# Kernel optimization log

Hardware: AMD Instinct MI355X
Metric: run time of the kernel (lower is better)

The kernel has to match this reference:

```python
import jax, jax.numpy as jnp
import numpy as np

ANG = 5  # angRes; n = ANG*ANG
EPS = 1e-12  # torch F.normalize eps

def _l2norm(x, axis):
    n = jnp.sqrt(jnp.sum(x * x, axis=axis, keepdims=True))
    return x / jnp.maximum(n, EPS)

def setup_inputs() -> dict:
    key = jax.random.key(0)
    kq, kk, kv = jax.random.split(key, 3)
    shape = (16, 16, 25, 16, 128)  # b c n h w
    return {
        "token_q": jax.random.normal(kq, shape, dtype=jnp.float32),
        "token_k": jax.random.normal(kk, shape, dtype=jnp.float32),
        "token_v": jax.random.normal(kv, shape, dtype=jnp.float32),
    }

def reference(token_q, token_k, token_v):
    b, c, n, h, w = token_q.shape
    u = v = ANG
    buffer = token_v

    def to_q(x):  # b c (u v) h w -> b (c h) (w u v)
        return x.reshape(b, c, u, v, h, w).transpose(0, 1, 4, 5, 2, 3).reshape(b, c * h, w * u * v)

    def to_k(x):  # b c (u v) h w -> b (w u v) (c h)
        return x.reshape(b, c, u, v, h, w).transpose(0, 5, 2, 3, 1, 4).reshape(b, w * u * v, c * h)

    unfold_q = _l2norm(to_q(token_q), axis=-1)      # [b, ch, wuv]
    unfold_k = _l2norm(to_k(token_k), axis=-2)      # [b, wuv, ch]
    unfold_v = to_q(token_v)                        # [b, ch, wuv]

    att = jnp.einsum('bts,bsr->btr', unfold_q, unfold_k)  # [b, ch, ch]
    size = c * h
    causal = jnp.tril(jnp.ones((size, size), dtype=bool))
    att = jnp.where(causal, att, jnp.float32(-1e15))
    att = jax.nn.softmax(att, axis=-1)

    out = jnp.einsum('btr,brs->bts', att, unfold_v)  # [b, ch, wuv]
    # b (c h) (w u v) -> b c (u v) h w
    out = out.reshape(b, c, h, w, u, v).transpose(0, 1, 4, 5, 2, 3).reshape(b, c, n, h, w)
    return out + buffer
```

## Files before the change

### kernel.cpp

```cpp
#include <hip/hip_runtime.h>
#include <math.h>

#define SB 819200
#define SC 51200
#define SN 2048
#define CH 256
#define NW 3200
#define NPARTS 10
#define PARTLEN 320
#define NCHUNK 5
#define SPART 1048576
#define G1BLOCKS 480

typedef __bf16 bf16x8 __attribute__((ext_vector_type(8)));
typedef __bf16 bf16x4 __attribute__((ext_vector_type(4)));
typedef __bf16 bf16x2 __attribute__((ext_vector_type(2)));
typedef float  f32x4  __attribute__((ext_vector_type(4)));

__device__ __forceinline__ bf16x8 cvt8(float4 a, float4 b) {
    bf16x8 r;
    r[0] = (__bf16)a.x; r[1] = (__bf16)a.y; r[2] = (__bf16)a.z; r[3] = (__bf16)a.w;
    r[4] = (__bf16)b.x; r[5] = (__bf16)b.y; r[6] = (__bf16)b.z; r[7] = (__bf16)b.w;
    return r;
}

__device__ __forceinline__ float dot4(float4 a) {
    return a.x * a.x + a.y * a.y + a.z * a.z + a.w * a.w;
}

__global__ __launch_bounds__(256, 2) void gemm1_kernel(const float* __restrict__ q,
                                                       const float* __restrict__ k,
                                                       float* __restrict__ Sp,
                                                       float* __restrict__ nq2p,
                                                       float* __restrict__ nk2p) {
    __shared__ alignas(16) __bf16 As[128 * 72];
    __shared__ alignas(16) __bf16 Bs[128 * 72];

    const int tid = threadIdx.x;
    const int lane = tid & 63;
    const int wave = tid >> 6;

    const int bx = blockIdx.x;
    const int tile = bx % 3;
    const int part = (bx / 3) % NPARTS;
    const int b = bx / (3 * NPARTS);
    const int tm = (tile + 1) >> 1;
    const int tn = tile >> 1;

    const int wm = wave >> 1;
    const int wn = wave & 1;

    const int srow = tid >> 1;
    const int scol = (tid & 1) * 32;
    const int ta = tm * 128 + srow;
    const int rb = tn * 128 + srow;
    const float* qrow = q + (size_t)b * SB + (size_t)(ta >> 4) * SC + (size_t)(ta & 15) * 128;
    const float* krow = k + (size_t)b * SB + (size_t)(rb >> 4) * SC + (size_t)(rb & 15) * 128;

    const bool doQ = (tile != 2);
    const bool doK = (tile != 1);

    f32x4 acc[4][4] = {};
    bool live[4][4];
#pragma unroll
    for (int mi = 0; mi < 4; mi++)
#pragma unroll
        for (int ni = 0; ni < 4; ni++)
            live[mi][ni] = (tn * 128 + wn * 64 + ni * 16) <= (tm * 128 + wm * 64 + mi * 16);

    float sqa = 0.f, sqb = 0.f;
    float4 av[8], bv[8];

    {
        const int kg = part * PARTLEN;
        const size_t koff = (size_t)(kg >> 7) * SN + (kg & 127) + scol;
#pragma unroll
        for (int j = 0; j < 8; j++) {
            av[j] = *(const float4*)(qrow + koff + j * 4);
            bv[j] = *(const float4*)(krow + koff + j * 4);
        }
#pragma unroll
        for (int j = 0; j < 4; j++) {
            *(bf16x8*)&As[srow * 72 + scol + j * 8] = cvt8(av[2 * j], av[2 * j + 1]);
            *(bf16x8*)&Bs[srow * 72 + scol + j * 8] = cvt8(bv[2 * j], bv[2 * j + 1]);
        }
        if (doQ) {
#pragma unroll
            for (int j = 0; j < 8; j++) sqa += dot4(av[j]);
        }
        if (doK) {
#pragma unroll
            for (int j = 0; j < 8; j++) sqb += dot4(bv[j]);
        }
    }
    __syncthreads();

    for (int ch = 0; ch < NCHUNK; ch++) {
        if (ch < NCHUNK - 1) {
            const int kg = part * PARTLEN + (ch + 1) * 64;
            const size_t koff = (size_t)(kg >> 7) * SN + (kg & 127) + scol;
#pragma unroll
            for (int j = 0; j < 8; j++) {
                av[j] = *(const float4*)(qrow + koff + j * 4);
                bv[j] = *(const float4*)(krow + koff + j * 4);
            }
        }
#pragma unroll
        for (int ks = 0; ks < 2; ks++) {
            const int ko = ks * 32 + (lane >> 4) * 8;
            bf16x8 af[4], bf[4];
#pragma unroll
            for (int mi = 0; mi < 4; mi++)
                af[mi] = *(const bf16x8*)&As[(wm * 64 + mi * 16 + (lane & 15)) * 72 + ko];
#pragma unroll
            for (int ni = 0; ni < 4; ni++)
                bf[ni] = *(const bf16x8*)&Bs[(wn * 64 + ni * 16 + (lane & 15)) * 72 + ko];
#pragma unroll
            for (int mi = 0; mi < 4; mi++)
#pragma unroll
                for (int ni = 0; ni < 4; ni++)
                    if (live[mi][ni])
                        acc[mi][ni] = __builtin_amdgcn_mfma_f32_16x16x32_bf16(
                            af[mi], bf[ni], acc[mi][ni], 0, 0, 0);
        }
        if (ch < NCHUNK - 1) {
            __syncthreads();
#pragma unroll
            for (int j = 0; j < 4; j++) {
                *(bf16x8*)&As[srow * 72 + scol + j * 8] = cvt8(av[2 * j], av[2 * j + 1]);
                *(bf16x8*)&Bs[srow * 72 + scol + j * 8] = cvt8(bv[2 * j], bv[2 * j + 1]);
            }
            if (doQ) {
#pragma unroll
                for (int j = 0; j < 8; j++) sqa += dot4(av[j]);
            }
            if (doK) {
#pragma unroll
                for (int j = 0; j < 8; j++) sqb += dot4(bv[j]);
            }
            __syncthreads();
        }
    }

    float* o = Sp + (size_t)part * SPART + (size_t)b * 65536;
#pragma unroll
    for (int mi = 0; mi < 4; mi++)
#pragma unroll
        for (int ni = 0; ni < 4; ni++) {
            if (!live[mi][ni]) continue;
            const int r = tn * 128 + wn * 64 + ni * 16 + (lane & 15);
#pragma unroll
            for (int j = 0; j < 4; j++) {
                const int t = tm * 128 + wm * 64 + mi * 16 + (lane >> 4) * 4 + j;
                o[(size_t)t * 256 + r] = acc[mi][ni][j];
            }
        }

    sqa += __shfl_xor(sqa, 1, 64);
    sqb += __shfl_xor(sqb, 1, 64);
    if (!(lane & 1)) {
        if (doQ) nq2p[part * 4096 + b * 256 + ta] = sqa;
        if (doK) nk2p[part * 4096 + b * 256 + rb] = sqb;
    }
}

__global__ __launch_bounds__(256) void softmax_kernel(const float* __restrict__ Sp,
                                                      const float* __restrict__ nq2p,
                                                      const float* __restrict__ nk2p,
                                                      __bf16* __restrict__ P) {
    const int wave = threadIdx.x >> 6;
    const int lane = threadIdx.x & 63;
    const int t = blockIdx.x * 4 + wave;
    const int b = blockIdx.y;
    const size_t rowbase = ((size_t)b * 256 + t) * 256;
    const int r0 = lane * 4;

    float4 s4 = {0.f, 0.f, 0.f, 0.f};
#pragma unroll
    for (int p = 0; p < NPARTS; p++) {
        const float4 x = *(const float4*)(Sp + (size_t)p * SPART + rowbase + r0);
        s4.x += x.x; s4.y += x.y; s4.z += x.z; s4.w += x.w;
    }
    float sq = 0.f;
#pragma unroll
    for (int p = 0; p < NPARTS; p++) sq += nq2p[p * 4096 + b * 256 + t];
    float4 sk = {0.f, 0.f, 0.f, 0.f};
#pragma unroll
    for (int p = 0; p < NPARTS; p++) {
        const float4 x = *(const float4*)(nk2p + p * 4096 + b * 256 + r0);
        sk.x += x.x; sk.y += x.y; sk.z += x.z; sk.w += x.w;
    }
    const float qn = 1.0f / fmaxf(sqrtf(sq), 1e-12f);
    float4 kn;
    kn.x = 1.0f / fmaxf(sqrtf(sk.x), 1e-12f);
    kn.y = 1.0f / fmaxf(sqrtf(sk.y), 1e-12f);
    kn.z = 1.0f / fmaxf(sqrtf(sk.z), 1e-12f);
    kn.w = 1.0f / fmaxf(sqrtf(sk.w), 1e-12f);

    float val[4] = {s4.x * qn * kn.x, s4.y * qn * kn.y,
                    s4.z * qn * kn.z, s4.w * qn * kn.w};
    float m = -1e30f;
#pragma unroll
    for (int j = 0; j < 4; j++) {
        if (r0 + j > t) val[j] = -1e30f;
        m = fmaxf(m, val[j]);
    }
#pragma unroll
    for (int off = 32; off; off >>= 1) m = fmaxf(m, __shfl_xor(m, off, 64));

    float e[4], sum = 0.f;
#pragma unroll
    for (int j = 0; j < 4; j++) {
        e[j] = (r0 + j <= t) ? expf(val[j] - m) : 0.f;
        sum += e[j];
    }
#pragma unroll
    for (int off = 32; off; off >>= 1) sum += __shfl_xor(sum, off, 64);

    const float inv = 1.0f / sum;
    bf16x4 o;
    o[0] = (__bf16)(e[0] * inv);
    o[1] = (__bf16)(e[1] * inv);
    o[2] = (__bf16)(e[2] * inv);
    o[3] = (__bf16)(e[3] * inv);
    *(bf16x4*)(P + rowbase + r0) = o;
}

__global__ __launch_bounds__(256, 4) void gemm2_kernel(const __bf16* __restrict__ P,
                                                       const float* __restrict__ v,
                                                       float* __restrict__ out) {
    __shared__ alignas(16) char smem[9216];
    __bf16* Vs = (__bf16*)smem;
    float* Es = (float*)smem;

    const int tid = threadIdx.x;
    const int b = blockIdx.z;
    const int tt = blockIdx.y;
    const int nw = blockIdx.x;
    const int n = nw >> 1;
    const int whalf = nw & 1;

    const int lane = tid & 63;
    const int wave = tid >> 6;
    const int wm = wave >> 1;
    const int wn = wave & 1;
    const int l15 = lane & 15;
    const int quad = lane >> 4;

    const int vu = tid & 7;
    const int rp = tid >> 3;
    const float* vbase = v + (size_t)b * SB + (size_t)n * SN + whalf * 64;

    const __bf16* Pbase = P + ((size_t)b * 256 + tt * 128 + wm * 64 + l15) * 256 + quad * 8;

    f32x4 acc[4][2] = {};

    for (int kc = 0; kc < 4; kc++) {
        bf16x8 af[4][2];
#pragma unroll
        for (int mi = 0; mi < 4; mi++)
#pragma unroll
            for (int ks = 0; ks < 2; ks++)
                af[mi][ks] = *(const bf16x8*)(Pbase + (size_t)mi * 16 * 256 + kc * 64 + ks * 32);

        float vr0[8], vr1[8];
        {
            const int r0 = kc * 64 + 2 * rp;
            const int r1 = r0 + 1;
            const float* row0 = vbase + (size_t)(r0 >> 4) * SC + (size_t)(r0 & 15) * 128;
            const float* row1 = vbase + (size_t)(r1 >> 4) * SC + (size_t)(r1 & 15) * 128;
            *(float4*)&vr0[0] = *(const float4*)(row0 + vu * 8);
            *(float4*)&vr0[4] = *(const float4*)(row0 + vu * 8 + 4);
            *(float4*)&vr1[0] = *(const float4*)(row1 + vu * 8);
            *(float4*)&vr1[4] = *(const float4*)(row1 + vu * 8 + 4);
        }
        __syncthreads();
        {
            const int rl0 = 2 * rp;
#pragma unroll
            for (int sj = 0; sj < 8; sj++) {
                const int s = vu * 8 + sj;
                bf16x2 pr;
                pr[0] = (__bf16)vr0[sj];
                pr[1] = (__bf16)vr1[sj];
                *(bf16x2*)&Vs[s * 72 + (rl0 ^ (s & 0x38))] = pr;
            }
        }
        __syncthreads();
#pragma unroll
        for (int ks = 0; ks < 2; ks++) {
            bf16x8 bfr[2];
#pragma unroll
            for (int ni = 0; ni < 2; ni++) {
                const int s = wn * 32 + ni * 16 + l15;
                bfr[ni] = *(const bf16x8*)&Vs[s * 72 + ((ks * 32 + quad * 8) ^ (s & 0x38))];
            }
#pragma unroll
            for (int mi = 0; mi < 4; mi++)
#pragma unroll
                for (int ni = 0; ni < 2; ni++)
                    acc[mi][ni] = __builtin_amdgcn_mfma_f32_16x16x32_bf16(
                        af[mi][ks], bfr[ni], acc[mi][ni], 0, 0, 0);
        }
    }

    for (int p = 0; p < 4; p++) {
        __syncthreads();
        if (wm == (p >> 1)) {
            const int mibase = (p & 1) * 2;
#pragma unroll
            for (int mm = 0; mm < 2; mm++)
#pragma unroll
                for (int ni = 0; ni < 2; ni++) {
                    const f32x4 a = acc[mibase + mm][ni];
                    const int wcol = wn * 32 + ni * 16 + l15;
#pragma unroll
                    for (int j = 0; j < 4; j++)
                        Es[(mm * 16 + quad * 4 + j) * 68 + wcol] = a[j];
                }
        }
        __syncthreads();
#pragma unroll
        for (int it = 0; it < 2; it++) {
            const int tl = it * 16 + (tid >> 4);
            const int w4 = (tid & 15) * 4;
            const int t = tt * 128 + p * 32 + tl;
            const size_t a = (size_t)b * SB + (size_t)(t >> 4) * SC + (size_t)n * SN +
                             (size_t)(t & 15) * 128 + whalf * 64 + w4;
            float4 r4 = *(const float4*)&Es[tl * 68 + w4];
            const float4 buf = *(const float4*)(v + a);
            r4.x += buf.x; r4.y += buf.y; r4.z += buf.z; r4.w += buf.w;
            *(float4*)(out + a) = r4;
        }
    }
}

extern "C" void kernel_launch(void* const* d_in, const int* in_sizes, int n_in,
                              void* d_out, int out_size, void* d_ws, size_t ws_size,
                              hipStream_t stream) {
    const float* q = (const float*)d_in[0];
    const float* k = (const float*)d_in[1];
    const float* v = (const float*)d_in[2];
    float* out = (float*)d_out;

    float* ws = (float*)d_ws;
    float* nq2p = ws;
    float* nk2p = ws + 40960;
    __bf16* P = (__bf16*)(ws + 81920);

    float* Spart = out;

    gemm1_kernel<<<dim3(G1BLOCKS), dim3(256), 0, stream>>>(q, k, Spart, nq2p, nk2p);
    softmax_kernel<<<dim3(64, 16), dim3(256), 0, stream>>>(Spart, nq2p, nk2p, P);
    gemm2_kernel<<<dim3(50, 2, 16), dim3(256), 0, stream>>>(P, v, out);
}
```

Baseline: 224.8 us.

## Stage gemm1 tiles via direct global-to-LDS loads with double buffering

The gemm1 kernel now copies fp32 tiles straight from global memory into LDS with global_load_lds, using two LDS buffers with a K-step of 32 and vmcnt waits so the next chunk loads while the current one computes. The fp32-to-bf16 conversion and the squared-norm sums move to the point where fragments are read from LDS, and a new shuffle reduction replaces the old norm write-out. The aim is to take register staging and conversion off the load path and overlap memory with MFMA. In exchange, LDS use doubles because it holds fp32, there are twice as many barriers, and reading fp32 from LDS may cause bank conflicts.

```diff
diff --git a/kernel.cpp b/kernel.cpp
--- a/kernel.cpp
+++ b/kernel.cpp
@@ -8,7 +8,8 @@
 #define NW 3200
 #define NPARTS 10
 #define PARTLEN 320
-#define NCHUNK 5
+#define BK 32
+#define NCH 10
 #define SPART 1048576
 #define G1BLOCKS 480
 
@@ -33,12 +34,13 @@
                                                        float* __restrict__ Sp,
                                                        float* __restrict__ nq2p,
                                                        float* __restrict__ nk2p) {
-    __shared__ alignas(16) __bf16 As[128 * 72];
-    __shared__ alignas(16) __bf16 Bs[128 * 72];
+    __shared__ alignas(16) float lds[16384];
 
     const int tid = threadIdx.x;
     const int lane = tid & 63;
     const int wave = tid >> 6;
+    const int l15 = lane & 15;
+    const int quad = lane >> 4;
 
     const int bx = blockIdx.x;
     const int tile = bx % 3;
@@ -50,16 +52,23 @@
     const int wm = wave >> 1;
     const int wn = wave & 1;
 
-    const int srow = tid >> 1;
-    const int scol = (tid & 1) * 32;
-    const int ta = tm * 128 + srow;
-    const int rb = tn * 128 + srow;
-    const float* qrow = q + (size_t)b * SB + (size_t)(ta >> 4) * SC + (size_t)(ta & 15) * 128;
-    const float* krow = k + (size_t)b * SB + (size_t)(rb >> 4) * SC + (size_t)(rb & 15) * 128;
-
     const bool doQ = (tile != 2);
     const bool doK = (tile != 1);
 
+    const int g8 = lane & 7;
+    const int rl = lane >> 3;
+
+    const float* qp[4];
+    const float* kp[4];
+#pragma unroll
+    for (int i = 0; i < 4; i++) {
+        const int row = wave * 32 + i * 8 + rl;
+        const int ta = tm * 128 + row;
+        const int rb = tn * 128 + row;
+        qp[i] = q + (size_t)b * SB + (size_t)(ta >> 4) * SC + (size_t)(ta & 15) * 128 + g8 * 4;
+        kp[i] = k + (size_t)b * SB + (size_t)(rb >> 4) * SC + (size_t)(rb & 15) * 128 + g8 * 4;
+    }
+
     f32x4 acc[4][4] = {};
     bool live[4][4];
 #pragma unroll
@@ -68,78 +77,67 @@
         for (int ni = 0; ni < 4; ni++)
             live[mi][ni] = (tn * 128 + wn * 64 + ni * 16) <= (tm * 128 + wm * 64 + mi * 16);
 
-    float sqa = 0.f, sqb = 0.f;
-    float4 av[8], bv[8];
-
-    {
-        const int kg = part * PARTLEN;
-        const size_t koff = (size_t)(kg >> 7) * SN + (kg & 127) + scol;
-#pragma unroll
-        for (int j = 0; j < 8; j++) {
-            av[j] = *(const float4*)(qrow + koff + j * 4);
-            bv[j] = *(const float4*)(krow + koff + j * 4);
-        }
-#pragma unroll
-        for (int j = 0; j < 4; j++) {
-            *(bf16x8*)&As[srow * 72 + scol + j * 8] = cvt8(av[2 * j], av[2 * j + 1]);
-            *(bf16x8*)&Bs[srow * 72 + scol + j * 8] = cvt8(bv[2 * j], bv[2 * j + 1]);
-        }
-        if (doQ) {
-#pragma unroll
-            for (int j = 0; j < 8; j++) sqa += dot4(av[j]);
-        }
-        if (doK) {
-#pragma unroll
-            for (int j = 0; j < 8; j++) sqb += dot4(bv[j]);
-        }
-    }
-    __syncthreads();
-
-    for (int ch = 0; ch < NCHUNK; ch++) {
-        if (ch < NCHUNK - 1) {
-            const int kg = part * PARTLEN + (ch + 1) * 64;
-            const size_t koff = (size_t)(kg >> 7) * SN + (kg & 127) + scol;
-#pragma unroll
-            for (int j = 0; j < 8; j++) {
-                av[j] = *(const float4*)(qrow + koff + j * 4);
-                bv[j] = *(const float4*)(krow + koff + j * 4);
-            }
-        }
-#pragma unroll
-        for (int ks = 0; ks < 2; ks++) {
-            const int ko = ks * 32 + (lane >> 4) * 8;
-            bf16x8 af[4], bf[4];
-#pragma unroll
-            for (int mi = 0; mi < 4; mi++)
-                af[mi] = *(const bf16x8*)&As[(wm * 64 + mi * 16 + (lane & 15)) * 72 + ko];
+    float sqA[4] = {0.f, 0.f, 0.f, 0.f};
+    float sqB[4] = {0.f, 0.f, 0.f, 0.f};
+
+    auto stage = [&](int ch, int p) {
+        const int kg = part * PARTLEN + ch * BK;
+        const size_t koff = (size_t)(kg >> 7) * SN + (kg & 127);
+#pragma unroll
+        for (int i = 0; i < 4; i++)
+            __builtin_amdgcn_global_load_lds(
+                (const __attribute__((address_space(1))) void*)(qp[i] + koff),
+                (__attribute__((address_space(3))) void*)(&lds[p * 8192 + (wave * 4 + i) * 256]),
+                16, 0, 0);
+#pragma unroll
+        for (int i = 0; i < 4; i++)
+            __builtin_amdgcn_global_load_lds(
+                (const __attribute__((address_space(1))) void*)(kp[i] + koff),
+                (__attribute__((address_space(3))) void*)(&lds[p * 8192 + 4096 + (wave * 4 + i) * 256]),
+                16, 0, 0);
+    };
+
+    stage(0, 0);
+
+    for (int ch = 0; ch < NCH; ch++) {
+        const int p = ch & 1;
+        if (ch + 1 < NCH) {
+            stage(ch + 1, 1 - p);
+            asm volatile("s_waitcnt vmcnt(8)" ::: "memory");
+        } else {
+            asm volatile("s_waitcnt vmcnt(0)" ::: "memory");
+        }
+        __builtin_amdgcn_s_barrier();
+        __builtin_amdgcn_sched_barrier(0);
+
+        const float* A = &lds[p * 8192];
+        const float* B = &lds[p * 8192 + 4096];
+        bf16x8 af[4], bfr[4];
+#pragma unroll
+        for (int mi = 0; mi < 4; mi++) {
+            const float4 lo = *(const float4*)&A[(wm * 64 + mi * 16 + l15) * 32 + quad * 8];
+            const float4 hi = *(const float4*)&A[(wm * 64 + mi * 16 + l15) * 32 + quad * 8 + 4];
+            af[mi] = cvt8(lo, hi);
+            if (wn == 0) sqA[mi] += dot4(lo) + dot4(hi);
+        }
+#pragma unroll
+        for (int ni = 0; ni < 4; ni++) {
+            const float4 lo = *(const float4*)&B[(wn * 64 + ni * 16 + l15) * 32 + quad * 8];
+            const float4 hi = *(const float4*)&B[(wn * 64 + ni * 16 + l15) * 32 + quad * 8 + 4];
+            bfr[ni] = cvt8(lo, hi);
+            if (wm == 0) sqB[ni] += dot4(lo) + dot4(hi);
+        }
+#pragma unroll
+        for (int mi = 0; mi < 4; mi++)
 #pragma unroll
             for (int ni = 0; ni < 4; ni++)
-                bf[ni] = *(const bf16x8*)&Bs[(wn * 64 + ni * 16 + (lane & 15)) * 72 + ko];
-#pragma unroll
-            for (int mi = 0; mi < 4; mi++)
-#pragma unroll
-                for (int ni = 0; ni < 4; ni++)
-                    if (live[mi][ni])
-                        acc[mi][ni] = __builtin_amdgcn_mfma_f32_16x16x32_bf16(
-                            af[mi], bf[ni], acc[mi][ni], 0, 0, 0);
-        }
-        if (ch < NCHUNK - 1) {
-            __syncthreads();
-#pragma unroll
-            for (int j = 0; j < 4; j++) {
-                *(bf16x8*)&As[srow * 72 + scol + j * 8] = cvt8(av[2 * j], av[2 * j + 1]);
-                *(bf16x8*)&Bs[srow * 72 + scol + j * 8] = cvt8(bv[2 * j], bv[2 * j + 1]);
-            }
-            if (doQ) {
-#pragma unroll
-                for (int j = 0; j < 8; j++) sqa += dot4(av[j]);
-            }
-            if (doK) {
-#pragma unroll
-                for (int j = 0; j < 8; j++) sqb += dot4(bv[j]);
-            }
-            __syncthreads();
-        }
+                if (live[mi][ni])
+                    acc[mi][ni] = __builtin_amdgcn_mfma_f32_16x16x32_bf16(
+                        af[mi], bfr[ni], acc[mi][ni], 0, 0, 0);
+
+        __builtin_amdgcn_sched_barrier(0);
+        __builtin_amdgcn_s_barrier();
+        __builtin_amdgcn_sched_barrier(0);
     }
 
     float* o = Sp + (size_t)part * SPART + (size_t)b * 65536;
@@ -148,19 +146,33 @@
 #pragma unroll
         for (int ni = 0; ni < 4; ni++) {
             if (!live[mi][ni]) continue;
-            const int r = tn * 128 + wn * 64 + ni * 16 + (lane & 15);
+            const int r = tn * 128 + wn * 64 + ni * 16 + l15;
 #pragma unroll
             for (int j = 0; j < 4; j++) {
-                const int t = tm * 128 + wm * 64 + mi * 16 + (lane >> 4) * 4 + j;
+                const int t = tm * 128 + wm * 64 + mi * 16 + quad * 4 + j;
                 o[(size_t)t * 256 + r] = acc[mi][ni][j];
             }
         }
 
-    sqa += __shfl_xor(sqa, 1, 64);
-    sqb += __shfl_xor(sqb, 1, 64);
-    if (!(lane & 1)) {
-        if (doQ) nq2p[part * 4096 + b * 256 + ta] = sqa;
-        if (doK) nk2p[part * 4096 + b * 256 + rb] = sqb;
+    if (wn == 0 && doQ) {
+#pragma unroll
+        for (int mi = 0; mi < 4; mi++) {
+            float s = sqA[mi];
+            s += __shfl_xor(s, 16, 64);
+            s += __shfl_xor(s, 32, 64);
+            if (lane < 16)
+                nq2p[part * 4096 + b * 256 + tm * 128 + wm * 64 + mi * 16 + lane] = s;
+        }
+    }
+    if (wm == 0 && doK) {
+#pragma unroll
+        for (int ni = 0; ni < 4; ni++) {
+            float s = sqB[ni];
+            s += __shfl_xor(s, 16, 64);
+            s += __shfl_xor(s, 32, 64);
+            if (lane < 16)
+                nk2p[part * 4096 + b * 256 + tn * 128 + wn * 64 + ni * 16 + lane] = s;
+        }
     }
 }
 
```

Measured after the change: 232.2 us. 1.03x slower.
